# Kernel optimization log

Measured on AMD Instinct MI355X. Metric: run time of the kernel, lower is better.

The kernel has to match this reference:

```python
import jax, jax.numpy as jnp
import numpy as np

B, S, E, D, V, H, NL = 16, 1024, 64, 256, 10000, 8, 3
HD = D // H


def _ln(x, g, b):
    m = jnp.mean(x, -1, keepdims=True)
    v = jnp.mean((x - m) ** 2, -1, keepdims=True)
    return (x - m) / jnp.sqrt(v + 1e-5) * g + b


def _mha(q_in, kv_in, in_w, in_b, out_w, out_b, causal):
    # torch nn.MultiheadAttention with packed in_proj [3D, D]
    d = q_in.shape[-1]
    q = q_in @ in_w[:d].T + in_b[:d]
    k = kv_in @ in_w[d:2 * d].T + in_b[d:2 * d]
    v = kv_in @ in_w[2 * d:].T + in_b[2 * d:]
    sp = lambda t: t.reshape(t.shape[0], t.shape[1], H, HD).transpose(0, 2, 1, 3)
    q, k, v = sp(q), sp(k), sp(v)
    s = jnp.einsum('bhqd,bhkd->bhqk', q, k) / jnp.float32(np.sqrt(HD))
    if causal:
        L = s.shape[-1]
        s = jnp.where(jnp.tril(jnp.ones((L, L), bool)), s, jnp.float32(-1e30))
    a = jax.nn.softmax(s, -1)
    o = jnp.einsum('bhqk,bhkd->bhqd', a, v).transpose(0, 2, 1, 3).reshape(q_in.shape[0], -1, d)
    return o @ out_w.T + out_b


def setup_inputs() -> dict:
    key = jax.random.key(0)
    ks = iter(jax.random.split(key, 40))
    n = lambda *sh: jax.random.normal(next(ks), sh, jnp.float32) * 0.05
    d = dict(
        tractovka=n(B, E), context=n(B, E), card=n(B, E),
        enc_w=n(3, D, E), enc_b=n(3, D),
        enc_ln_g=jnp.ones((3, D), jnp.float32), enc_ln_b=jnp.zeros((3, D), jnp.float32),
        fusion_w=n(D, 3 * D), fusion_b=n(D),
        fusion_ln_g=jnp.ones(D, jnp.float32), fusion_ln_b=jnp.zeros(D, jnp.float32),
        tok_emb=n(V, D), pos_emb=n(1024, D),
        sa_in_w=n(NL, 3 * D, D), sa_in_b=n(NL, 3 * D), sa_out_w=n(NL, D, D), sa_out_b=n(NL, D),
        ca_in_w=n(NL, 3 * D, D), ca_in_b=n(NL, 3 * D), ca_out_w=n(NL, D, D), ca_out_b=n(NL, D),
        ln1_g=jnp.ones((NL, D), jnp.float32), ln1_b=jnp.zeros((NL, D), jnp.float32),
        ln2_g=jnp.ones((NL, D), jnp.float32), ln2_b=jnp.zeros((NL, D), jnp.float32),
        ln3_g=jnp.ones((NL, D), jnp.float32), ln3_b=jnp.zeros((NL, D), jnp.float32),
        ffn_w1=n(NL, 4 * D, D), ffn_b1=n(NL, 4 * D), ffn_w2=n(NL, D, 4 * D), ffn_b2=n(NL, D),
        out_w=n(V, D), out_b=n(V),
        prev_tokens=jax.random.randint(next(ks), (B, S), 0, V, jnp.int32),
    )
    return d


def reference(tractovka, context, card, enc_w, enc_b, enc_ln_g, enc_ln_b,
              fusion_w, fusion_b, fusion_ln_g, fusion_ln_b, tok_emb, pos_emb,
              sa_in_w, sa_in_b, sa_out_w, sa_out_b, ca_in_w, ca_in_b, ca_out_w, ca_out_b,
              ln1_g, ln1_b, ln2_g, ln2_b, ln3_g, ln3_b,
              ffn_w1, ffn_b1, ffn_w2, ffn_b2, out_w, out_b, prev_tokens):
    enc = lambda x, i: jax.nn.gelu(_ln(x @ enc_w[i].T + enc_b[i], enc_ln_g[i], enc_ln_b[i]), approximate=False)
    mem = jnp.concatenate([enc(tractovka, 0), enc(context, 1), enc(card, 2)], -1)
    mem = jax.nn.gelu(_ln(mem @ fusion_w.T + fusion_b, fusion_ln_g, fusion_ln_b), approximate=False)[:, None, :]  # [B,1,D]
    x = tok_emb[prev_tokens] + pos_emb[:prev_tokens.shape[1]][None]  # [B,S,D]
    for i in range(NL):  # post-norm decoder layer: self-attn, cross-attn, ReLU FFN
        x = _ln(x + _mha(x, x, sa_in_w[i], sa_in_b[i], sa_out_w[i], sa_out_b[i], True), ln1_g[i], ln1_b[i])
        x = _ln(x + _mha(x, mem, ca_in_w[i], ca_in_b[i], ca_out_w[i], ca_out_b[i], False), ln2_g[i], ln2_b[i])
        x = _ln(x + (jax.nn.relu(x @ ffn_w1[i].T + ffn_b1[i]) @ ffn_w2[i].T + ffn_b2[i]), ln3_g[i], ln3_b[i])
    return x @ out_w.T + out_b  # [B,S,V]
```

## Files before the change

### kernel.cpp

```cpp
#include <hip/hip_runtime.h>
#include <math.h>

constexpr int B = 16, S = 1024, D = 256, E = 64, H = 8, HD = 32;

typedef __attribute__((ext_vector_type(8))) short bf16x8;
typedef __attribute__((ext_vector_type(4))) short bf16x4;
typedef __attribute__((ext_vector_type(4))) float f32x4;

__device__ __forceinline__ float gelu_f(float x) {
  return 0.5f * x * (1.0f + erff(x * 0.70710678118654752440f));
}

__device__ __forceinline__ unsigned short f2bf(float f) {
  union { float f; unsigned u; } x; x.f = f;
  unsigned r = x.u + 0x7fff + ((x.u >> 16) & 1);
  return (unsigned short)(r >> 16);
}

__device__ __forceinline__ unsigned cvt_pk_bf16(float a, float b) {
  unsigned r;
  asm("v_cvt_pk_bf16_f32 %0, %1, %2" : "=v"(r) : "v"(a), "v"(b));
  return r;
}

__device__ __forceinline__ void gl16(const void* g, void* l) {
  __builtin_amdgcn_global_load_lds(
      (const __attribute__((address_space(1))) void*)g,
      (__attribute__((address_space(3))) void*)l, 16, 0, 0);
}

__global__ void k_cvt_all(const float* __restrict__ s0, const float* __restrict__ s1,
                          const float* __restrict__ s2, const float* __restrict__ s3,
                          const float* __restrict__ s4, unsigned short* __restrict__ dst) {
  int i = (blockIdx.x * 256 + threadIdx.x) * 4;
  const float* src;
  int off;
  if (i < 589824)       { src = s0; off = i; }
  else if (i < 786432)  { src = s1; off = i - 589824; }
  else if (i < 1572864) { src = s2; off = i - 786432; }
  else if (i < 2359296) { src = s3; off = i - 1572864; }
  else                  { src = s4; off = i - 2359296; }
  float4 v = *(const float4*)(src + off);
  dst[i + 0] = f2bf(v.x);
  dst[i + 1] = f2bf(v.y);
  dst[i + 2] = f2bf(v.z);
  dst[i + 3] = f2bf(v.w);
}

__global__ void k_embed(const int* __restrict__ tok,
                        const float* __restrict__ tok_emb,
                        const float* __restrict__ pos_emb,
                        float* __restrict__ x, unsigned short* __restrict__ xb) {
  int t = threadIdx.x;
  int r = blockIdx.x * 4 + (t >> 6);
  int c4 = (t & 63) * 4;
  int s = r & (S - 1);
  int tk = tok[r];
  float4 te = *(const float4*)(tok_emb + (size_t)tk * D + c4);
  float4 pe = *(const float4*)(pos_emb + (size_t)s * D + c4);
  float4 v = make_float4(te.x + pe.x, te.y + pe.y, te.z + pe.z, te.w + pe.w);
  *(float4*)(x + (size_t)r * D + c4) = v;
  unsigned lo = cvt_pk_bf16(v.x, v.y), hi = cvt_pk_bf16(v.z, v.w);
  *(uint2*)(xb + (size_t)r * D + c4) = make_uint2(lo, hi);
}

__global__ __launch_bounds__(256)
void k_side(const float* __restrict__ tr, const float* __restrict__ ctx,
            const float* __restrict__ card,
            const float* __restrict__ enc_w, const float* __restrict__ enc_b,
            const float* __restrict__ eg, const float* __restrict__ ebt,
            const float* __restrict__ fw, const float* __restrict__ fb,
            const float* __restrict__ fg, const float* __restrict__ fbt,
            const float* __restrict__ ca_in_w, const float* __restrict__ ca_in_b,
            const float* __restrict__ ca_out_w, const float* __restrict__ ca_out_b,
            float* __restrict__ ca_add) {
  int b = blockIdx.x, d = threadIdx.x;
  __shared__ float catl[768], meml[256], vs[256];
  __shared__ float rw1[4], rw2[4];

  auto lnstat = [&](float acc, float& mean, float& rstd) {
    float a1 = acc, a2 = acc * acc;
#pragma unroll
    for (int off = 32; off > 0; off >>= 1) {
      a1 += __shfl_xor(a1, off);
      a2 += __shfl_xor(a2, off);
    }
    int wid = d >> 6, lane = d & 63;
    if (lane == 0) { rw1[wid] = a1; rw2[wid] = a2; }
    __syncthreads();
    float s1 = rw1[0] + rw1[1] + rw1[2] + rw1[3];
    float s2 = rw2[0] + rw2[1] + rw2[2] + rw2[3];
    mean = s1 * (1.0f / D);
    float var = s2 * (1.0f / D) - mean * mean;
    rstd = rsqrtf(var + 1e-5f);
    __syncthreads();
  };

  for (int i = 0; i < 3; ++i) {
    const float* xin = (i == 0 ? tr : (i == 1 ? ctx : card)) + b * E;
    const float* wr = enc_w + ((size_t)i * D + d) * E;
    float acc = enc_b[i * D + d];
#pragma unroll 8
    for (int e = 0; e < E; ++e) acc += xin[e] * wr[e];
    float mean, rstd;
    lnstat(acc, mean, rstd);
    float nv = (acc - mean) * rstd * eg[i * D + d] + ebt[i * D + d];
    catl[i * D + d] = gelu_f(nv);
  }
  __syncthreads();

  {
    const float* fwr = fw + (size_t)d * 768;
    float fa = fb[d];
    for (int k = 0; k < 768; ++k) fa += catl[k] * fwr[k];
    float mean, rstd;
    lnstat(fa, mean, rstd);
    meml[d] = gelu_f((fa - mean) * rstd * fg[d] + fbt[d]);
  }
  __syncthreads();

  for (int l = 0; l < 3; ++l) {
    const float* wi = ca_in_w + ((size_t)l * 768 + 512 + d) * 256;
    float v = ca_in_b[l * 768 + 512 + d];
    for (int k = 0; k < 256; ++k) v += meml[k] * wi[k];
    vs[d] = v;
    __syncthreads();
    const float* wo = ca_out_w + ((size_t)l * 256 + d) * 256;
    float o = ca_out_b[l * 256 + d];
    for (int k = 0; k < 256; ++k) o += vs[k] * wo[k];
    ca_add[((size_t)l * B + b) * 256 + d] = o;
    __syncthreads();
  }
}

__global__ __launch_bounds__(512)
void k_attn6(const unsigned short* __restrict__ qkv, unsigned short* __restrict__ out) {
  constexpr int KT = 64;
  __shared__ unsigned short Ks[2][KT * 32];
  __shared__ unsigned short Vt[2][32 * KT];
  __shared__ unsigned short Pl[8 * 32 * KT];

  const int t = threadIdx.x;
  const int w = t >> 6, lane = t & 63;
  const int lg = lane >> 4, lr = lane & 15;
  const int bh = blockIdx.y;
  const int h = bh & (H - 1), b = bh >> 3;
  const int qtile = (int)gridDim.x - 1 - (int)blockIdx.x;
  const int qb = qtile << 8;
  const int qw = qb + w * 32;
  const unsigned short* base = qkv + (size_t)b * S * 768 + h * HD;

  bf16x8 qf[2];
#pragma unroll
  for (int qr = 0; qr < 2; ++qr)
    qf[qr] = *(const bf16x8*)(base + (size_t)(qw + qr * 16 + lr) * 768 + lg * 8);

  f32x4 o[2][2];
#pragma unroll
  for (int qr = 0; qr < 2; ++qr)
#pragma unroll
    for (int dt = 0; dt < 2; ++dt) o[qr][dt] = (f32x4){0.f, 0.f, 0.f, 0.f};
  float mq[2], lq[2];
#pragma unroll
  for (int qr = 0; qr < 2; ++qr) { mq[qr] = -3.0e38f; lq[qr] = 0.f; }

  const float Cs = 0.17677669529663687f * 1.4426950408889634f;

  const int skey = t >> 2;
  const int sch = (t & 3) * 8;
  const int vkey = t >> 3;
  const int vch = (t & 7) * 4;
  char* pbase = (char*)Pl + (w << 12);

  const int nkt = (qb + 256) >> 6;

  if (t < 256) gl16(base + (size_t)skey * 768 + 256 + sch, (char*)Ks[0] + t * 16);
  bf16x4 vv = *(const bf16x4*)(base + (size_t)vkey * 768 + 512 + vch);
  __syncthreads();

  for (int kti = 0; kti < nkt; ++kti) {
    const int kt = kti << 6;
    const int cur = kti & 1;

#pragma unroll
    for (int j = 0; j < 4; ++j) {
      int d = vch + j;
      int byteo = d * (KT * 2) + ((vkey * 2) ^ ((d & 7) << 4));
      *(unsigned short*)((char*)Vt[cur] + byteo) = (unsigned short)vv[j];
    }
    if (kti + 1 < nkt) {
      if (t < 256)
        gl16(base + (size_t)(kt + KT + skey) * 768 + 256 + sch, (char*)Ks[cur ^ 1] + t * 16);
      vv = *(const bf16x4*)(base + (size_t)(kt + KT + vkey) * 768 + 512 + vch);
    }

    const bool active = (kt <= qw + 31);
    if (active) {
      bf16x8 kf[4];
#pragma unroll
      for (int t4 = 0; t4 < 4; ++t4)
        kf[t4] = *(const bf16x8*)&Ks[cur][(t4 * 16 + lr) * 32 + lg * 8];
      f32x4 sc[2][4];
      __builtin_amdgcn_s_setprio(1);
#pragma unroll
      for (int qr = 0; qr < 2; ++qr)
#pragma unroll
        for (int t4 = 0; t4 < 4; ++t4)
          sc[qr][t4] = __builtin_amdgcn_mfma_f32_16x16x32_bf16(
              kf[t4], qf[qr], (f32x4){0.f, 0.f, 0.f, 0.f}, 0, 0, 0);
      __builtin_amdgcn_s_setprio(0);

      if (kt + KT > qw) {
#pragma unroll
        for (int qr = 0; qr < 2; ++qr) {
          int q = qw + qr * 16 + lr;
#pragma unroll
          for (int t4 = 0; t4 < 4; ++t4)
#pragma unroll
            for (int r = 0; r < 4; ++r) {
              int k = kt + t4 * 16 + lg * 4 + r;
              if (k > q) sc[qr][t4][r] = -3.0e38f;
            }
        }
      }

#pragma unroll
      for (int qr = 0; qr < 2; ++qr) {
        float mx = sc[qr][0][0];
#pragma unroll
        for (int t4 = 0; t4 < 4; ++t4)
#pragma unroll
          for (int r = 0; r < 4; ++r) mx = fmaxf(mx, sc[qr][t4][r]);
        mx = fmaxf(mx, __shfl_xor(mx, 16));
        mx = fmaxf(mx, __shfl_xor(mx, 32));
        if (__any(mx > mq[qr] + 8.0f)) {
          float mn = fmaxf(mx, mq[qr]);
          float cf = exp2f((mq[qr] - mn) * Cs);
          mq[qr] = mn;
          lq[qr] *= cf;
#pragma unroll
          for (int r = 0; r < 4; ++r) {
            float cfo = __shfl(cf, (lane & 48) | (lg * 4 + r));
            o[qr][0][r] *= cfo;
            o[qr][1][r] *= cfo;
          }
        }
        float nmxC = -mq[qr] * Cs;
        float ps = 0.f;
#pragma unroll
        for (int t4 = 0; t4 < 4; ++t4)
#pragma unroll
          for (int r = 0; r < 4; ++r) {
            float p = exp2f(fmaf(sc[qr][t4][r], Cs, nmxC));
            sc[qr][t4][r] = p;
            ps += p;
          }
        lq[qr] += ps;
        int ql = qr * 16 + lr;
        int swz = (ql & 7) << 4;
        char* prow = pbase + ql * (KT * 2);
#pragma unroll
        for (int t4 = 0; t4 < 4; ++t4) {
          unsigned lo = cvt_pk_bf16(sc[qr][t4][0], sc[qr][t4][1]);
          unsigned hi = cvt_pk_bf16(sc[qr][t4][2], sc[qr][t4][3]);
          *(uint2*)(prow + ((t4 * 32 + lg * 8) ^ swz)) = make_uint2(lo, hi);
        }
      }
    }

    __syncthreads();

    if (active) {
#pragma unroll
      for (int kp = 0; kp < 2; ++kp) {
        bf16x8 vf[2], pf[2];
        int kb = kp * 64 + lg * 16;
#pragma unroll
        for (int dt = 0; dt < 2; ++dt) {
          int d = dt * 16 + lr;
          vf[dt] = *(const bf16x8*)((char*)Vt[cur] + d * (KT * 2) + (kb ^ ((d & 7) << 4)));
        }
#pragma unroll
        for (int qr = 0; qr < 2; ++qr) {
          int ql = qr * 16 + lr;
          pf[qr] = *(const bf16x8*)(pbase + ql * (KT * 2) + (kb ^ ((ql & 7) << 4)));
        }
        __builtin_amdgcn_s_setprio(1);
#pragma unroll
        for (int qr = 0; qr < 2; ++qr)
#pragma unroll
          for (int dt = 0; dt < 2; ++dt)
            o[qr][dt] = __builtin_amdgcn_mfma_f32_16x16x32_bf16(
                pf[qr], vf[dt], o[qr][dt], 0, 0, 0);
        __builtin_amdgcn_s_setprio(0);
      }
    }
  }

#pragma unroll
  for (int qr = 0; qr < 2; ++qr) {
    float ls = lq[qr];
    ls += __shfl_xor(ls, 16);
    ls += __shfl_xor(ls, 32);
    float invq = 1.0f / ls;
#pragma unroll
    for (int r = 0; r < 4; ++r) {
      float inv = __shfl(invq, (lane & 48) | (lg * 4 + r));
      int q = qw + qr * 16 + lg * 4 + r;
      unsigned short* orow = out + (size_t)(b * S + q) * D + h * HD;
#pragma unroll
      for (int dt = 0; dt < 2; ++dt)
        orow[dt * 16 + lr] = f2bf(o[qr][dt][r] * inv);
    }
  }
}

template <int EPI, int OUTBF, int SWZ>
__global__ __launch_bounds__(256)
void k_gemm_mfma(const unsigned short* __restrict__ A,
                 const unsigned short* __restrict__ W,
                 const float* __restrict__ bias,
                 void* __restrict__ Cout,
                 int M, int N, int K) {
  __shared__ unsigned short As[128][32];
  __shared__ unsigned short Bs[128][32];
  int t = threadIdx.x;
  int bx = blockIdx.x, by = blockIdx.y;
  if (SWZ) {
    int nx = gridDim.x;
    int lin = by * nx + bx;
    int q = (nx * (int)gridDim.y) >> 3;
    int nl = (lin & 7) * q + (lin >> 3);
    by = nl / nx;
    bx = nl - by * nx;
  }
  int row0 = by * 128, col0 = bx * 128;
  int wid = t >> 6, lane = t & 63;
  int wr = wid >> 1, wc = wid & 1;
  int lrow = lane & 15, lko = (lane >> 4) * 8;

  f32x4 acc[4][4];
#pragma unroll
  for (int mi = 0; mi < 4; ++mi)
#pragma unroll
    for (int ni = 0; ni < 4; ++ni)
      acc[mi][ni] = (f32x4){0.f, 0.f, 0.f, 0.f};

  int c0 = t, c1 = t + 256;
  int ar0 = c0 >> 2, aq0 = (c0 & 3) * 8;
  int ar1 = c1 >> 2, aq1 = (c1 & 3) * 8;
  int wrow0 = col0 + ar0; if (wrow0 > N - 1) wrow0 = N - 1;
  int wrow1 = col0 + ar1; if (wrow1 > N - 1) wrow1 = N - 1;

  const unsigned short* A0 = A + (size_t)(row0 + ar0) * K + aq0;
  const unsigned short* A1 = A + (size_t)(row0 + ar1) * K + aq1;
  const unsigned short* W0 = W + (size_t)wrow0 * K + aq0;
  const unsigned short* W1 = W + (size_t)wrow1 * K + aq1;

  for (int kt = 0; kt < K; kt += 32) {
    gl16(A0 + kt, (char*)As + c0 * 16);
    gl16(A1 + kt, (char*)As + c1 * 16);
    gl16(W0 + kt, (char*)Bs + c0 * 16);
    gl16(W1 + kt, (char*)Bs + c1 * 16);
    __syncthreads();

    bf16x8 af[4], bfr[4];
#pragma unroll
    for (int mi = 0; mi < 4; ++mi)
      af[mi] = *(const bf16x8*)&As[wr * 64 + mi * 16 + lrow][lko];
#pragma unroll
    for (int ni = 0; ni < 4; ++ni)
      bfr[ni] = *(const bf16x8*)&Bs[wc * 64 + ni * 16 + lrow][lko];
#pragma unroll
    for (int mi = 0; mi < 4; ++mi)
#pragma unroll
      for (int ni = 0; ni < 4; ++ni)
        acc[mi][ni] = __builtin_amdgcn_mfma_f32_16x16x32_bf16(af[mi], bfr[ni], acc[mi][ni], 0, 0, 0);
    __syncthreads();
  }

  int rbase = row0 + wr * 64 + (lane >> 4) * 4;
  int cbase = col0 + wc * 64 + lrow;
#pragma unroll
  for (int ni = 0; ni < 4; ++ni) {
    int c = cbase + ni * 16;
    if (c < N) {
      float bv = bias[c];
#pragma unroll
      for (int mi = 0; mi < 4; ++mi) {
        int rr = rbase + mi * 16;
#pragma unroll
        for (int r = 0; r < 4; ++r) {
          float v = acc[mi][ni][r] + bv;
          if (EPI == 1) v = fmaxf(v, 0.0f);
          size_t off = (size_t)(rr + r) * N + c;
          if (OUTBF)
            ((unsigned short*)Cout)[off] = f2bf(v);
          else
            ((float*)Cout)[off] = v;
        }
      }
    }
  }
}

template <int NLN>
__global__ __launch_bounds__(256)
void k_gemm_ln(const unsigned short* __restrict__ A,
               const unsigned short* __restrict__ W,
               const float* __restrict__ bias,
               const float* __restrict__ res,
               const float* __restrict__ ca,
               const float* __restrict__ g1, const float* __restrict__ b1,
               const float* __restrict__ g2, const float* __restrict__ b2,
               float* __restrict__ xout, unsigned short* __restrict__ xb,
               int K) {
  __shared__ unsigned short As[4][64][32];
  __shared__ unsigned short Bs[4][256][32];
  __shared__ float red[2][64][4];
  int t = threadIdx.x;
  int row0 = blockIdx.x * 64;
  int wc = t >> 6, lane = t & 63;
  int lr = lane & 15, lg = lane >> 4;

  f32x4 acc[4][4];
#pragma unroll
  for (int mi = 0; mi < 4; ++mi)
#pragma unroll
    for (int ni = 0; ni < 4; ++ni)
      acc[mi][ni] = (f32x4){0.f, 0.f, 0.f, 0.f};

  int arw = t >> 2, aq = (t & 3) * 8;
  const unsigned short* srcA = A + (size_t)(row0 + arw) * K + aq;
  int adoff = t * 16;
  const unsigned short* srcB[4];
  int bdoff[4];
#pragma unroll
  for (int j = 0; j < 4; ++j) {
    int cb = t + (j << 8);
    int rw = cb >> 2, q = (cb & 3) * 8;
    srcB[j] = W + (size_t)rw * K + q;
    bdoff[j] = cb * 16;
  }

  auto stage = [&](int s) {
    int slot = s & 3;
    int off = s << 5;
    gl16(srcA + off, (char*)As[slot] + adoff);
#pragma unroll
    for (int j = 0; j < 4; ++j) gl16(srcB[j] + off, (char*)Bs[slot] + bdoff[j]);
  };

  const int nsteps = K >> 5;
  stage(0);
  stage(1);
  for (int s = 0; s < nsteps; ++s) {
    if (s + 2 < nsteps) {
      stage(s + 2);
      asm volatile("s_waitcnt vmcnt(10)" ::: "memory");
    } else if (s + 1 < nsteps) {
      asm volatile("s_waitcnt vmcnt(5)" ::: "memory");
    } else {
      asm volatile("s_waitcnt vmcnt(0)" ::: "memory");
    }
    __builtin_amdgcn_s_barrier();
    __builtin_amdgcn_sched_barrier(0);
    int slot = s & 3;
    bf16x8 af[4], bfr[4];
#pragma unroll
    for (int mi = 0; mi < 4; ++mi)
      af[mi] = *(const bf16x8*)&As[slot][mi * 16 + lr][lg * 8];
#pragma unroll
    for (int ni = 0; ni < 4; ++ni)
      bfr[ni] = *(const bf16x8*)&Bs[slot][wc * 64 + ni * 16 + lr][lg * 8];
    __builtin_amdgcn_s_setprio(1);
#pragma unroll
    for (int mi = 0; mi < 4; ++mi)
#pragma unroll
      for (int ni = 0; ni < 4; ++ni)
        acc[mi][ni] = __builtin_amdgcn_mfma_f32_16x16x32_bf16(af[mi], bfr[ni], acc[mi][ni], 0, 0, 0);
    __builtin_amdgcn_s_setprio(0);
  }

  int colb = wc * 64 + lr;
  float mean[4][4], rstd[4][4];

#pragma unroll
  for (int mi = 0; mi < 4; ++mi) {
#pragma unroll
    for (int r = 0; r < 4; ++r) {
      int rowl = mi * 16 + lg * 4 + r;
      int rowg = row0 + rowl;
      float s1 = 0.f, s2 = 0.f;
#pragma unroll
      for (int ni = 0; ni < 4; ++ni) {
        int c = colb + ni * 16;
        float v = acc[mi][ni][r] + bias[c] + res[(size_t)rowg * D + c];
        acc[mi][ni][r] = v;
        s1 += v; s2 += v * v;
      }
#pragma unroll
      for (int msk = 1; msk <= 8; msk <<= 1) {
        s1 += __shfl_xor(s1, msk);
        s2 += __shfl_xor(s2, msk);
      }
      if (lr == 0) { red[0][rowl][wc] = s1; red[1][rowl][wc] = s2; }
    }
  }
  __syncthreads();
#pragma unroll
  for (int mi = 0; mi < 4; ++mi)
#pragma unroll
    for (int r = 0; r < 4; ++r) {
      int rowl = mi * 16 + lg * 4 + r;
      f32x4 a = *(const f32x4*)&red[0][rowl][0];
      f32x4 bq = *(const f32x4*)&red[1][rowl][0];
      float s1 = a[0] + a[1] + a[2] + a[3];
      float s2 = bq[0] + bq[1] + bq[2] + bq[3];
      float mn = s1 * (1.0f / D);
      float vr = s2 * (1.0f / D) - mn * mn;
      mean[mi][r] = mn;
      rstd[mi][r] = rsqrtf(vr + 1e-5f);
    }
#pragma unroll
  for (int mi = 0; mi < 4; ++mi)
#pragma unroll
    for (int ni = 0; ni < 4; ++ni) {
      int c = colb + ni * 16;
      float gg = g1[c], bb = b1[c];
#pragma unroll
      for (int r = 0; r < 4; ++r)
        acc[mi][ni][r] = (acc[mi][ni][r] - mean[mi][r]) * rstd[mi][r] * gg + bb;
    }

  if (NLN == 2) {
    __syncthreads();
#pragma unroll
    for (int mi = 0; mi < 4; ++mi) {
#pragma unroll
      for (int r = 0; r < 4; ++r) {
        int rowl = mi * 16 + lg * 4 + r;
        int rowg = row0 + rowl;
        int bidx = rowg >> 10;
        float s1 = 0.f, s2 = 0.f;
#pragma unroll
        for (int ni = 0; ni < 4; ++ni) {
          int c = colb + ni * 16;
          float v = acc[mi][ni][r] + ca[(size_t)bidx * D + c];
          acc[mi][ni][r] = v;
          s1 += v; s2 += v * v;
        }
#pragma unroll
        for (int msk = 1; msk <= 8; msk <<= 1) {
          s1 += __shfl_xor(s1, msk);
          s2 += __shfl_xor(s2, msk);
        }
        if (lr == 0) { red[0][rowl][wc] = s1; red[1][rowl][wc] = s2; }
      }
    }
    __syncthreads();
#pragma unroll
    for (int mi = 0; mi < 4; ++mi)
#pragma unroll
      for (int r = 0; r < 4; ++r) {
        int rowl = mi * 16 + lg * 4 + r;
        f32x4 a = *(const f32x4*)&red[0][rowl][0];
        f32x4 bq = *(const f32x4*)&red[1][rowl][0];
        float s1 = a[0] + a[1] + a[2] + a[3];
        float s2 = bq[0] + bq[1] + bq[2] + bq[3];
        float mn = s1 * (1.0f / D);
        float vr = s2 * (1.0f / D) - mn * mn;
        mean[mi][r] = mn;
        rstd[mi][r] = rsqrtf(vr + 1e-5f);
      }
#pragma unroll
    for (int mi = 0; mi < 4; ++mi)
#pragma unroll
      for (int ni = 0; ni < 4; ++ni) {
        int c = colb + ni * 16;
        float gg = g2[c], bb = b2[c];
#pragma unroll
        for (int r = 0; r < 4; ++r)
          acc[mi][ni][r] = (acc[mi][ni][r] - mean[mi][r]) * rstd[mi][r] * gg + bb;
      }
  }

#pragma unroll
  for (int mi = 0; mi < 4; ++mi)
#pragma unroll
    for (int r = 0; r < 4; ++r) {
      int rowg = row0 + mi * 16 + lg * 4 + r;
#pragma unroll
      for (int ni = 0; ni < 4; ++ni) {
        int c = colb + ni * 16;
        float v = acc[mi][ni][r];
        xout[(size_t)rowg * D + c] = v;
        xb[(size_t)rowg * D + c] = f2bf(v);
      }
    }
}

extern "C" void kernel_launch(void* const* d_in, const int* in_sizes, int n_in,
                              void* d_out, int out_size, void* d_ws, size_t ws_size,
                              hipStream_t stream) {
  (void)in_sizes; (void)n_in; (void)out_size; (void)ws_size;
  const float* tractovka = (const float*)d_in[0];
  const float* context   = (const float*)d_in[1];
  const float* card      = (const float*)d_in[2];
  const float* enc_w     = (const float*)d_in[3];
  const float* enc_b     = (const float*)d_in[4];
  const float* enc_ln_g  = (const float*)d_in[5];
  const float* enc_ln_b  = (const float*)d_in[6];
  const float* fusion_w  = (const float*)d_in[7];
  const float* fusion_b  = (const float*)d_in[8];
  const float* fusion_ln_g = (const float*)d_in[9];
  const float* fusion_ln_b = (const float*)d_in[10];
  const float* tok_emb   = (const float*)d_in[11];
  const float* pos_emb   = (const float*)d_in[12];
  const float* sa_in_w   = (const float*)d_in[13];
  const float* sa_in_b   = (const float*)d_in[14];
  const float* sa_out_w  = (const float*)d_in[15];
  const float* sa_out_b  = (const float*)d_in[16];
  const float* ca_in_w   = (const float*)d_in[17];
  const float* ca_in_b   = (const float*)d_in[18];
  const float* ca_out_w  = (const float*)d_in[19];
  const float* ca_out_b  = (const float*)d_in[20];
  const float* ln1_g     = (const float*)d_in[21];
  const float* ln1_b     = (const float*)d_in[22];
  const float* ln2_g     = (const float*)d_in[23];
  const float* ln2_b     = (const float*)d_in[24];
  const float* ln3_g     = (const float*)d_in[25];
  const float* ln3_b     = (const float*)d_in[26];
  const float* ffn_w1    = (const float*)d_in[27];
  const float* ffn_b1    = (const float*)d_in[28];
  const float* ffn_w2    = (const float*)d_in[29];
  const float* ffn_b2    = (const float*)d_in[30];
  const float* out_w     = (const float*)d_in[31];
  const float* out_b     = (const float*)d_in[32];
  const int*   prev      = (const int*)d_in[33];
  float* out = (float*)d_out;

  const int M = B * S;

  float* ws = (float*)d_ws;
  float* x      = ws;
  float* bufA   = x + (size_t)M * D;
  float* bufB   = bufA + (size_t)M * 768;
  float* cat    = bufB + (size_t)M * D;
  float* mem    = cat + (size_t)B * 3 * D;
  float* ca_add = mem + (size_t)B * D;
  unsigned short* xb    = (unsigned short*)(ca_add + (size_t)3 * B * D);
  unsigned short* attnb = xb + (size_t)M * D;
  unsigned short* wbf   = attnb + (size_t)M * D;
  unsigned short* qkvb  = (unsigned short*)bufA;
  unsigned short* ffn1b = (unsigned short*)bufA;

  const int n_qkvw = 3 * 768 * D;
  const int n_outw = 3 * D * D;
  const int n_f1w  = 3 * 1024 * D;
  const int n_f2w  = 3 * D * 1024;
  unsigned short* w_qkv = wbf;
  unsigned short* w_out = w_qkv + n_qkvw;
  unsigned short* w_f1  = w_out + n_outw;
  unsigned short* w_f2  = w_f1 + n_f1w;
  unsigned short* w_v   = w_f2 + n_f2w;

  k_cvt_all<<<4804, 256, 0, stream>>>(sa_in_w, sa_out_w, ffn_w1, ffn_w2, out_w, wbf);

  k_embed<<<M / 4, 256, 0, stream>>>(prev, tok_emb, pos_emb, x, xb);
  k_side<<<B, 256, 0, stream>>>(tractovka, context, card,
                                enc_w, enc_b, enc_ln_g, enc_ln_b,
                                fusion_w, fusion_b, fusion_ln_g, fusion_ln_b,
                                ca_in_w, ca_in_b, ca_out_w, ca_out_b, ca_add);

  for (int l = 0; l < 3; ++l) {
    k_gemm_mfma<0, 1, 0><<<dim3(6, M / 128), 256, 0, stream>>>(
        xb, w_qkv + (size_t)l * 768 * D, sa_in_b + (size_t)l * 3 * D, qkvb,
        M, 768, D);
    k_attn6<<<dim3(S / 256, B * H), 512, 0, stream>>>(qkvb, attnb);
    k_gemm_ln<2><<<dim3(M / 64), 256, 0, stream>>>(
        attnb, w_out + (size_t)l * D * D, sa_out_b + (size_t)l * D,
        x, ca_add + (size_t)l * B * D,
        ln1_g + (size_t)l * D, ln1_b + (size_t)l * D,
        ln2_g + (size_t)l * D, ln2_b + (size_t)l * D,
        x, xb, D);
    k_gemm_mfma<1, 1, 0><<<dim3(8, M / 128), 256, 0, stream>>>(
        xb, w_f1 + (size_t)l * 1024 * D, ffn_b1 + (size_t)l * 4 * D, ffn1b,
        M, 1024, D);
    k_gemm_ln<1><<<dim3(M / 64), 256, 0, stream>>>(
        ffn1b, w_f2 + (size_t)l * D * 1024, ffn_b2 + (size_t)l * D,
        x, nullptr,
        ln3_g + (size_t)l * D, ln3_b + (size_t)l * D,
        nullptr, nullptr,
        x, xb, 1024);
  }
  k_gemm_mfma<0, 0, 1><<<dim3(79, M / 128), 256, 0, stream>>>(
      xb, w_v, out_b, out, M, 10000, D);
}
```

Measured before the change: 825.6 us.

## Halve row tile of fused GEMM+LayerNorm kernel and simplify to double buffering

The fused output-projection/FFN2 GEMM with LayerNorm epilogue now processes 32 rows per block instead of 64, doubling the grid to 512 blocks. The intent is to fill more of the chip's compute units, since the old 256-block grid left many idle. The four-slot prefetch pipeline with manual vmcnt waits is replaced by a simple two-slot double buffer synchronized with __syncthreads, and only half the threads load A. The trade-off is that each block now reads the full 256-column weight tile for half as many rows, so weight reuse drops, and the shallower pipeline hides less load latency.

```diff
diff --git a/kernel.cpp b/kernel.cpp
--- a/kernel.cpp
+++ b/kernel.cpp
@@ -415,24 +415,28 @@
                const float* __restrict__ g2, const float* __restrict__ b2,
                float* __restrict__ xout, unsigned short* __restrict__ xb,
                int K) {
-  __shared__ unsigned short As[4][64][32];
-  __shared__ unsigned short Bs[4][256][32];
-  __shared__ float red[2][64][4];
+  __shared__ unsigned short As[2][32][32];
+  __shared__ unsigned short Bs[2][256][32];
+  __shared__ float red[2][32][4];
   int t = threadIdx.x;
-  int row0 = blockIdx.x * 64;
+  int row0 = blockIdx.x * 32;
   int wc = t >> 6, lane = t & 63;
   int lr = lane & 15, lg = lane >> 4;
 
-  f32x4 acc[4][4];
-#pragma unroll
-  for (int mi = 0; mi < 4; ++mi)
+  f32x4 acc[2][4];
+#pragma unroll
+  for (int mi = 0; mi < 2; ++mi)
 #pragma unroll
     for (int ni = 0; ni < 4; ++ni)
       acc[mi][ni] = (f32x4){0.f, 0.f, 0.f, 0.f};
 
-  int arw = t >> 2, aq = (t & 3) * 8;
-  const unsigned short* srcA = A + (size_t)(row0 + arw) * K + aq;
-  int adoff = t * 16;
+  const unsigned short* srcA = nullptr;
+  int adoff = 0;
+  if (t < 128) {
+    int rw = t >> 2, q = (t & 3) * 8;
+    srcA = A + (size_t)(row0 + rw) * K + q;
+    adoff = t * 16;
+  }
   const unsigned short* srcB[4];
   int bdoff[4];
 #pragma unroll
@@ -443,50 +447,42 @@
     bdoff[j] = cb * 16;
   }
 
-  auto stage = [&](int s) {
-    int slot = s & 3;
-    int off = s << 5;
-    gl16(srcA + off, (char*)As[slot] + adoff);
-#pragma unroll
-    for (int j = 0; j < 4; ++j) gl16(srcB[j] + off, (char*)Bs[slot] + bdoff[j]);
-  };
-
   const int nsteps = K >> 5;
-  stage(0);
-  stage(1);
+  if (t < 128) gl16(srcA, (char*)As[0] + adoff);
+#pragma unroll
+  for (int j = 0; j < 4; ++j) gl16(srcB[j], (char*)Bs[0] + bdoff[j]);
+  __syncthreads();
+
   for (int s = 0; s < nsteps; ++s) {
-    if (s + 2 < nsteps) {
-      stage(s + 2);
-      asm volatile("s_waitcnt vmcnt(10)" ::: "memory");
-    } else if (s + 1 < nsteps) {
-      asm volatile("s_waitcnt vmcnt(5)" ::: "memory");
-    } else {
-      asm volatile("s_waitcnt vmcnt(0)" ::: "memory");
-    }
-    __builtin_amdgcn_s_barrier();
-    __builtin_amdgcn_sched_barrier(0);
-    int slot = s & 3;
-    bf16x8 af[4], bfr[4];
-#pragma unroll
-    for (int mi = 0; mi < 4; ++mi)
-      af[mi] = *(const bf16x8*)&As[slot][mi * 16 + lr][lg * 8];
+    const int cur = s & 1;
+    if (s + 1 < nsteps) {
+      int off = (s + 1) << 5;
+      if (t < 128) gl16(srcA + off, (char*)As[cur ^ 1] + adoff);
+#pragma unroll
+      for (int j = 0; j < 4; ++j) gl16(srcB[j] + off, (char*)Bs[cur ^ 1] + bdoff[j]);
+    }
+    bf16x8 af[2], bfr[4];
+#pragma unroll
+    for (int mi = 0; mi < 2; ++mi)
+      af[mi] = *(const bf16x8*)&As[cur][mi * 16 + lr][lg * 8];
 #pragma unroll
     for (int ni = 0; ni < 4; ++ni)
-      bfr[ni] = *(const bf16x8*)&Bs[slot][wc * 64 + ni * 16 + lr][lg * 8];
+      bfr[ni] = *(const bf16x8*)&Bs[cur][wc * 64 + ni * 16 + lr][lg * 8];
     __builtin_amdgcn_s_setprio(1);
 #pragma unroll
-    for (int mi = 0; mi < 4; ++mi)
+    for (int mi = 0; mi < 2; ++mi)
 #pragma unroll
       for (int ni = 0; ni < 4; ++ni)
         acc[mi][ni] = __builtin_amdgcn_mfma_f32_16x16x32_bf16(af[mi], bfr[ni], acc[mi][ni], 0, 0, 0);
     __builtin_amdgcn_s_setprio(0);
+    __syncthreads();
   }
 
   int colb = wc * 64 + lr;
-  float mean[4][4], rstd[4][4];
-
-#pragma unroll
-  for (int mi = 0; mi < 4; ++mi) {
+  float mean[2][4], rstd[2][4];
+
+#pragma unroll
+  for (int mi = 0; mi < 2; ++mi) {
 #pragma unroll
     for (int r = 0; r < 4; ++r) {
       int rowl = mi * 16 + lg * 4 + r;
@@ -509,7 +505,7 @@
   }
   __syncthreads();
 #pragma unroll
-  for (int mi = 0; mi < 4; ++mi)
+  for (int mi = 0; mi < 2; ++mi)
 #pragma unroll
     for (int r = 0; r < 4; ++r) {
       int rowl = mi * 16 + lg * 4 + r;
@@ -523,7 +519,7 @@
       rstd[mi][r] = rsqrtf(vr + 1e-5f);
     }
 #pragma unroll
-  for (int mi = 0; mi < 4; ++mi)
+  for (int mi = 0; mi < 2; ++mi)
 #pragma unroll
     for (int ni = 0; ni < 4; ++ni) {
       int c = colb + ni * 16;
@@ -536,7 +532,7 @@
   if (NLN == 2) {
     __syncthreads();
 #pragma unroll
-    for (int mi = 0; mi < 4; ++mi) {
+    for (int mi = 0; mi < 2; ++mi) {
 #pragma unroll
       for (int r = 0; r < 4; ++r) {
         int rowl = mi * 16 + lg * 4 + r;
@@ -560,7 +556,7 @@
     }
     __syncthreads();
 #pragma unroll
-    for (int mi = 0; mi < 4; ++mi)
+    for (int mi = 0; mi < 2; ++mi)
 #pragma unroll
       for (int r = 0; r < 4; ++r) {
         int rowl = mi * 16 + lg * 4 + r;
@@ -574,7 +570,7 @@
         rstd[mi][r] = rsqrtf(vr + 1e-5f);
       }
 #pragma unroll
-    for (int mi = 0; mi < 4; ++mi)
+    for (int mi = 0; mi < 2; ++mi)
 #pragma unroll
       for (int ni = 0; ni < 4; ++ni) {
         int c = colb + ni * 16;
@@ -586,7 +582,7 @@
   }
 
 #pragma unroll
-  for (int mi = 0; mi < 4; ++mi)
+  for (int mi = 0; mi < 2; ++mi)
 #pragma unroll
     for (int r = 0; r < 4; ++r) {
       int rowg = row0 + mi * 16 + lg * 4 + r;
@@ -678,7 +674,7 @@
         xb, w_qkv + (size_t)l * 768 * D, sa_in_b + (size_t)l * 3 * D, qkvb,
         M, 768, D);
     k_attn6<<<dim3(S / 256, B * H), 512, 0, stream>>>(qkvb, attnb);
-    k_gemm_ln<2><<<dim3(M / 64), 256, 0, stream>>>(
+    k_gemm_ln<2><<<dim3(M / 32), 256, 0, stream>>>(
         attnb, w_out + (size_t)l * D * D, sa_out_b + (size_t)l * D,
         x, ca_add + (size_t)l * B * D,
         ln1_g + (size_t)l * D, ln1_b + (size_t)l * D,
@@ -687,7 +683,7 @@
     k_gemm_mfma<1, 1, 0><<<dim3(8, M / 128), 256, 0, stream>>>(
         xb, w_f1 + (size_t)l * 1024 * D, ffn_b1 + (size_t)l * 4 * D, ffn1b,
         M, 1024, D);
-    k_gemm_ln<1><<<dim3(M / 64), 256, 0, stream>>>(
+    k_gemm_ln<1><<<dim3(M / 32), 256, 0, stream>>>(
         ffn1b, w_f2 + (size_t)l * D * 1024, ffn_b2 + (size_t)l * D,
         x, nullptr,
         ln3_g + (size_t)l * D, ln3_b + (size_t)l * D,
```

New measurement: 806.8 us. -2.3%, faster.
